# Performance work log

Hardware: AMD Instinct MI355X
Metric: run time of the kernel (lower is better)

The kernel has to match this reference:

```python
import jax, jax.numpy as jnp
import numpy as np

B, S, D_IN, D_A, L = 4, 4000, 1024, 512, 8921


def setup_inputs() -> dict:
    key = jax.random.key(0)
    ks = jax.random.split(key, 6)
    scale_w = 1.0 / np.sqrt(D_IN)
    scale_u = 1.0 / np.sqrt(D_A)
    return {
        "x": jax.random.normal(ks[0], (B, S, D_IN), jnp.float32),
        "W_w": jax.random.normal(ks[1], (D_A, D_IN), jnp.float32) * scale_w,
        "W_b": jax.random.normal(ks[2], (D_A,), jnp.float32) * 0.01,
        "U_w": jax.random.normal(ks[3], (L, D_A), jnp.float32) * scale_u,
        "V_w": jax.random.normal(ks[4], (L, D_A), jnp.float32) * scale_u,
        "V_b": jax.random.normal(ks[5], (L,), jnp.float32) * 0.01,
    }


def reference(x, W_w, W_b, U_w, V_w, V_b):
    # z = tanh(W x): [B, S, D_A]
    z = jnp.tanh(jnp.einsum("bsd,ad->bsa", x, W_w) + W_b)
    # label-wise attention scores over sequence: [B, L, S]
    scores = jnp.einsum("la,bsa->bls", U_w, z)
    alpha = jax.nn.softmax(scores, axis=-1)
    # per-label context vectors: [B, L, D_A]
    m = jnp.einsum("bls,bsa->bla", alpha, z)
    # per-label weighted dot-product classifier: [B, L]
    y = jnp.einsum("la,bla->bl", V_w, m) + V_b
    return (y, alpha)
```

## Files before the change

kernel.cpp:

```cpp
#include <hip/hip_runtime.h>
#include <hip/hip_bf16.h>
#include <math.h>

#define B_   4
#define S_   4000
#define DIN  1024
#define DA   512
#define L_   8921

typedef __attribute__((ext_vector_type(8))) short    short8;
typedef __attribute__((ext_vector_type(4))) float    f4;
typedef __attribute__((ext_vector_type(4))) unsigned int u4;

static __device__ __forceinline__ unsigned short f2b(float f) {
    unsigned int u = __float_as_uint(f);
    u += 0x7fffu + ((u >> 16) & 1u);
    return (unsigned short)(u >> 16);
}
static __device__ __forceinline__ unsigned int pack2(float lo, float hi) {
    return (unsigned int)f2b(lo) | ((unsigned int)f2b(hi) << 16);
}

__global__ __launch_bounds__(256) void k_z(const float* __restrict__ x,
                                           const float* __restrict__ Ww,
                                           const float* __restrict__ Wb,
                                           unsigned short* __restrict__ z)
{
    __shared__ unsigned short lds_a[128 * 32];
    __shared__ unsigned short lds_b[128 * 32];

    const int tid  = threadIdx.x;
    const int lane = tid & 63;
    const int w    = tid >> 6;
    const int wm   = w >> 1, wn = w & 1;
    const int q    = lane >> 4, r = lane & 15;
    const int m0   = blockIdx.x * 128;
    const int n0   = blockIdx.y * 128;

    f4 acc[4][4];
#pragma unroll
    for (int i = 0; i < 4; i++)
#pragma unroll
        for (int j = 0; j < 4; j++) { f4 zz = {0.f,0.f,0.f,0.f}; acc[i][j] = zz; }

    const int row  = tid >> 1;
    const int half = tid & 1;

    for (int kk = 0; kk < DIN; kk += 32) {
        {
            const f4* src = (const f4*)(x + (size_t)(m0 + row) * DIN + kk + half * 16);
            f4 v0 = src[0], v1 = src[1], v2 = src[2], v3 = src[3];
            u4* dst = (u4*)&lds_a[row * 32 + half * 16];
            u4 o0, o1;
            o0[0] = pack2(v0[0], v0[1]); o0[1] = pack2(v0[2], v0[3]);
            o0[2] = pack2(v1[0], v1[1]); o0[3] = pack2(v1[2], v1[3]);
            o1[0] = pack2(v2[0], v2[1]); o1[1] = pack2(v2[2], v2[3]);
            o1[2] = pack2(v3[0], v3[1]); o1[3] = pack2(v3[2], v3[3]);
            dst[0] = o0; dst[1] = o1;
        }
        {
            const f4* src = (const f4*)(Ww + (size_t)(n0 + row) * DIN + kk + half * 16);
            f4 v0 = src[0], v1 = src[1], v2 = src[2], v3 = src[3];
            u4* dst = (u4*)&lds_b[row * 32 + half * 16];
            u4 o0, o1;
            o0[0] = pack2(v0[0], v0[1]); o0[1] = pack2(v0[2], v0[3]);
            o0[2] = pack2(v1[0], v1[1]); o0[3] = pack2(v1[2], v1[3]);
            o1[0] = pack2(v2[0], v2[1]); o1[1] = pack2(v2[2], v2[3]);
            o1[2] = pack2(v3[0], v3[1]); o1[3] = pack2(v3[2], v3[3]);
            dst[0] = o0; dst[1] = o1;
        }
        __syncthreads();

        short8 af[4], bfr[4];
#pragma unroll
        for (int i = 0; i < 4; i++) {
            af[i]  = *(const short8*)&lds_a[(wm * 64 + i * 16 + r) * 32 + q * 8];
            bfr[i] = *(const short8*)&lds_b[(wn * 64 + i * 16 + r) * 32 + q * 8];
        }
#pragma unroll
        for (int i = 0; i < 4; i++)
#pragma unroll
            for (int j = 0; j < 4; j++)
                acc[i][j] = __builtin_amdgcn_mfma_f32_16x16x32_bf16(af[i], bfr[j], acc[i][j], 0, 0, 0);
        __syncthreads();
    }

#pragma unroll
    for (int i = 0; i < 4; i++) {
#pragma unroll
        for (int j = 0; j < 4; j++) {
            const int col = n0 + wn * 64 + j * 16 + r;
            const float bias = Wb[col];
#pragma unroll
            for (int e = 0; e < 4; e++) {
                const int rowg = m0 + wm * 64 + i * 16 + q * 4 + e;
                z[(size_t)rowg * DA + col] = f2b(tanhf(acc[i][j][e] + bias));
            }
        }
    }
}

__global__ __launch_bounds__(256) void k_scores(const float* __restrict__ U,
                                                const unsigned short* __restrict__ z,
                                                float* __restrict__ out)
{
    __shared__ unsigned short lds_a[128 * 32];
    __shared__ unsigned short lds_b[128 * 32];

    const int tid  = threadIdx.x;
    const int lane = tid & 63;
    const int w    = tid >> 6;
    const int wm   = w >> 1, wn = w & 1;
    const int q    = lane >> 4, r = lane & 15;
    const int b    = blockIdx.z;
    const int m0   = blockIdx.x * 128;
    const int n0   = blockIdx.y * 128;

    f4 acc[4][4];
#pragma unroll
    for (int i = 0; i < 4; i++)
#pragma unroll
        for (int j = 0; j < 4; j++) { f4 zz = {0.f,0.f,0.f,0.f}; acc[i][j] = zz; }

    const int row  = tid >> 1;
    const int half = tid & 1;
    const int brow = tid >> 2;
    const int bseg = tid & 3;

    for (int kk = 0; kk < DA; kk += 32) {
        {
            u4* dst = (u4*)&lds_a[row * 32 + half * 16];
            const int gm = m0 + row;
            if (gm < L_) {
                const f4* src = (const f4*)(U + (size_t)gm * DA + kk + half * 16);
                f4 v0 = src[0], v1 = src[1], v2 = src[2], v3 = src[3];
                u4 o0, o1;
                o0[0] = pack2(v0[0], v0[1]); o0[1] = pack2(v0[2], v0[3]);
                o0[2] = pack2(v1[0], v1[1]); o0[3] = pack2(v1[2], v1[3]);
                o1[0] = pack2(v2[0], v2[1]); o1[1] = pack2(v2[2], v2[3]);
                o1[2] = pack2(v3[0], v3[1]); o1[3] = pack2(v3[2], v3[3]);
                dst[0] = o0; dst[1] = o1;
            } else {
                u4 zz = {0,0,0,0}; dst[0] = zz; dst[1] = zz;
            }
        }
#pragma unroll
        for (int jj = 0; jj < 2; jj++) {
            const int rr = brow + jj * 64;
            const int gs = n0 + rr;
            u4* dst = (u4*)&lds_b[rr * 32 + bseg * 8];
            if (gs < S_) {
                *dst = *(const u4*)&z[((size_t)(b * S_ + gs)) * DA + kk + bseg * 8];
            } else {
                u4 zz = {0,0,0,0}; *dst = zz;
            }
        }
        __syncthreads();

        short8 af[4], bfr[4];
#pragma unroll
        for (int i = 0; i < 4; i++) {
            af[i]  = *(const short8*)&lds_a[(wm * 64 + i * 16 + r) * 32 + q * 8];
            bfr[i] = *(const short8*)&lds_b[(wn * 64 + i * 16 + r) * 32 + q * 8];
        }
#pragma unroll
        for (int i = 0; i < 4; i++)
#pragma unroll
            for (int j = 0; j < 4; j++)
                acc[i][j] = __builtin_amdgcn_mfma_f32_16x16x32_bf16(af[i], bfr[j], acc[i][j], 0, 0, 0);
        __syncthreads();
    }

#pragma unroll
    for (int i = 0; i < 4; i++) {
#pragma unroll
        for (int j = 0; j < 4; j++) {
            const int colg = n0 + wn * 64 + j * 16 + r;
#pragma unroll
            for (int e = 0; e < 4; e++) {
                const int rowg = m0 + wm * 64 + i * 16 + q * 4 + e;
                if (rowg < L_ && colg < S_)
                    out[((size_t)b * L_ + rowg) * S_ + colg] = acc[i][j][e];
            }
        }
    }
}

__global__ __launch_bounds__(256) void k_softmax(float* __restrict__ a)
{
    float* p = a + (size_t)blockIdx.x * S_;
    const int tid = threadIdx.x;

    f4 v[4];
    float mx = -3.4e38f;
#pragma unroll
    for (int j = 0; j < 4; j++) {
        const int vi = tid + j * 256;
        if (vi < S_ / 4) {
            v[j] = ((const f4*)p)[vi];
            mx = fmaxf(mx, fmaxf(fmaxf(v[j][0], v[j][1]), fmaxf(v[j][2], v[j][3])));
        }
    }
#pragma unroll
    for (int off = 32; off > 0; off >>= 1) mx = fmaxf(mx, __shfl_xor(mx, off, 64));

    __shared__ float red[8];
    if ((tid & 63) == 0) red[tid >> 6] = mx;
    __syncthreads();
    mx = fmaxf(fmaxf(red[0], red[1]), fmaxf(red[2], red[3]));

    float s = 0.f;
#pragma unroll
    for (int j = 0; j < 4; j++) {
        const int vi = tid + j * 256;
        if (vi < S_ / 4) {
#pragma unroll
            for (int c = 0; c < 4; c++) { v[j][c] = __expf(v[j][c] - mx); s += v[j][c]; }
        }
    }
#pragma unroll
    for (int off = 32; off > 0; off >>= 1) s += __shfl_xor(s, off, 64);
    if ((tid & 63) == 0) red[4 + (tid >> 6)] = s;
    __syncthreads();
    s = red[4] + red[5] + red[6] + red[7];

    const float inv = 1.f / s;
#pragma unroll
    for (int j = 0; j < 4; j++) {
        const int vi = tid + j * 256;
        if (vi < S_ / 4) {
            f4 o = v[j]; o[0] *= inv; o[1] *= inv; o[2] *= inv; o[3] *= inv;
            ((f4*)p)[vi] = o;
        }
    }
}

__global__ __launch_bounds__(256) void k_transpose(const unsigned short* __restrict__ z,
                                                   unsigned short* __restrict__ zT)
{
    __shared__ unsigned short t[32][33];
    const int b  = blockIdx.z;
    const int s0 = blockIdx.x * 32;
    const int a0 = blockIdx.y * 32;
    const int c  = threadIdx.x & 31;
    const int r4 = threadIdx.x >> 5;

#pragma unroll
    for (int i = 0; i < 4; i++) {
        const int sl = r4 * 4 + i;
        t[sl][c] = z[((size_t)(b * S_ + s0 + sl)) * DA + a0 + c];
    }
    __syncthreads();
#pragma unroll
    for (int i = 0; i < 4; i++) {
        const int al = r4 * 4 + i;
        zT[((size_t)(b * DA + a0 + al)) * S_ + s0 + c] = t[c][al];
    }
}

__global__ __launch_bounds__(256) void k_mv(const float* __restrict__ alpha,
                                            const unsigned short* __restrict__ zT,
                                            const float* __restrict__ Vw,
                                            const float* __restrict__ Vb,
                                            float* __restrict__ y)
{
    __shared__ unsigned short lds_a[64 * 32];
    __shared__ unsigned short lds_b[512 * 32];
    __shared__ float yred[64];

    const int tid  = threadIdx.x;
    const int lane = tid & 63;
    const int w    = tid >> 6;
    const int q    = lane >> 4, r = lane & 15;
    const int b    = blockIdx.y;
    const int m0   = blockIdx.x * 64;

    if (tid < 64) yred[tid] = 0.f;

    f4 acc[4][8];
#pragma unroll
    for (int i = 0; i < 4; i++)
#pragma unroll
        for (int j = 0; j < 8; j++) { f4 zz = {0.f,0.f,0.f,0.f}; acc[i][j] = zz; }

    const int arow = tid >> 2;
    const int aseg = tid & 3;

    for (int kk = 0; kk < S_; kk += 32) {
        {
            u4* dst = (u4*)&lds_a[arow * 32 + aseg * 8];
            const int gl = m0 + arow;
            if (gl < L_) {
                const f4* src = (const f4*)(alpha + ((size_t)b * L_ + gl) * S_ + kk + aseg * 8);
                f4 v0 = src[0], v1 = src[1];
                u4 o;
                o[0] = pack2(v0[0], v0[1]); o[1] = pack2(v0[2], v0[3]);
                o[2] = pack2(v1[0], v1[1]); o[3] = pack2(v1[2], v1[3]);
                *dst = o;
            } else {
                u4 zz = {0,0,0,0}; *dst = zz;
            }
        }
#pragma unroll
        for (int jj = 0; jj < 8; jj++) {
            const int rr = arow + jj * 64;
            *(u4*)&lds_b[rr * 32 + aseg * 8] =
                *(const u4*)&zT[((size_t)(b * DA + rr)) * S_ + kk + aseg * 8];
        }
        __syncthreads();

        short8 af[4], bfr[8];
#pragma unroll
        for (int i = 0; i < 4; i++)
            af[i] = *(const short8*)&lds_a[(i * 16 + r) * 32 + q * 8];
#pragma unroll
        for (int j = 0; j < 8; j++)
            bfr[j] = *(const short8*)&lds_b[(w * 128 + j * 16 + r) * 32 + q * 8];
#pragma unroll
        for (int i = 0; i < 4; i++)
#pragma unroll
            for (int j = 0; j < 8; j++)
                acc[i][j] = __builtin_amdgcn_mfma_f32_16x16x32_bf16(af[i], bfr[j], acc[i][j], 0, 0, 0);
        __syncthreads();
    }

#pragma unroll
    for (int i = 0; i < 4; i++) {
#pragma unroll
        for (int e = 0; e < 4; e++) {
            const int rowl = i * 16 + q * 4 + e;
            const int gl = m0 + rowl;
            if (gl < L_) {
                float p = 0.f;
#pragma unroll
                for (int j = 0; j < 8; j++) {
                    const int col = w * 128 + j * 16 + r;
                    p += acc[i][j][e] * Vw[(size_t)gl * DA + col];
                }
                atomicAdd(&yred[rowl], p);
            }
        }
    }
    __syncthreads();
    if (tid < 64 && (m0 + tid) < L_)
        y[b * L_ + m0 + tid] = yred[tid] + Vb[m0 + tid];
}

extern "C" void kernel_launch(void* const* d_in, const int* in_sizes, int n_in,
                              void* d_out, int out_size, void* d_ws, size_t ws_size,
                              hipStream_t stream)
{
    const float* x  = (const float*)d_in[0];
    const float* Ww = (const float*)d_in[1];
    const float* Wb = (const float*)d_in[2];
    const float* Uw = (const float*)d_in[3];
    const float* Vw = (const float*)d_in[4];
    const float* Vb = (const float*)d_in[5];

    float* y     = (float*)d_out;
    float* alpha = y + (size_t)B_ * L_;

    unsigned short* z  = (unsigned short*)d_ws;
    unsigned short* zT = z + (size_t)B_ * S_ * DA;

    k_z<<<dim3(125, 4), dim3(256), 0, stream>>>(x, Ww, Wb, z);
    k_scores<<<dim3(70, 32, B_), dim3(256), 0, stream>>>(Uw, z, alpha);
    k_softmax<<<dim3(B_ * L_), dim3(256), 0, stream>>>(alpha);
    k_transpose<<<dim3(125, 16, B_), dim3(256), 0, stream>>>(z, zT);
    k_mv<<<dim3(140, B_), dim3(256), 0, stream>>>(alpha, zT, Vw, Vb, y);
}
```

Before: 1.942 ms.

## Compute y via V·z scores and fuse softmax with the weighted reduction

The label outputs are rewritten algebraically as y[l] = Σ_s alpha[l,s]·(V_l·z_s) instead of first forming the context vectors m = alpha·z. A new GEMM kernel computes the U·z scores and the V·z products together, sharing the z tile loads, with U and V converted to bf16 beforehand. A fused kernel then does the softmax and the weighted sum over s in one pass, which removes the transpose and matrix-vector kernels. The catch is a full B×L×S intermediate (fp32, or bf16 as a fallback) that must be written and read back. This path only runs when the workspace is large enough; otherwise the old kernels are used.

```diff
diff --git a/kernel.cpp b/kernel.cpp
--- a/kernel.cpp
+++ b/kernel.cpp
@@ -8,9 +8,10 @@
 #define DA   512
 #define L_   8921
 
-typedef __attribute__((ext_vector_type(8))) short    short8;
-typedef __attribute__((ext_vector_type(4))) float    f4;
-typedef __attribute__((ext_vector_type(4))) unsigned int u4;
+typedef __attribute__((ext_vector_type(8))) short          short8;
+typedef __attribute__((ext_vector_type(4))) float          f4;
+typedef __attribute__((ext_vector_type(4))) unsigned int   u4;
+typedef __attribute__((ext_vector_type(4))) unsigned short us4;
 
 static __device__ __forceinline__ unsigned short f2b(float f) {
     unsigned int u = __float_as_uint(f);
@@ -19,6 +20,9 @@
 }
 static __device__ __forceinline__ unsigned int pack2(float lo, float hi) {
     return (unsigned int)f2b(lo) | ((unsigned int)f2b(hi) << 16);
+}
+static __device__ __forceinline__ float b2f(unsigned short u) {
+    return __uint_as_float(((unsigned int)u) << 16);
 }
 
 __global__ __launch_bounds__(256) void k_z(const float* __restrict__ x,
@@ -97,6 +101,180 @@
                 z[(size_t)rowg * DA + col] = f2b(tanhf(acc[i][j][e] + bias));
             }
         }
+    }
+}
+
+__global__ __launch_bounds__(256) void k_cvt(const float* __restrict__ src,
+                                             unsigned short* __restrict__ dst, int n8)
+{
+    const int i = blockIdx.x * 256 + threadIdx.x;
+    if (i < n8) {
+        const f4* s = (const f4*)src + (size_t)i * 2;
+        const f4 a = s[0], b = s[1];
+        u4 o;
+        o[0] = pack2(a[0], a[1]); o[1] = pack2(a[2], a[3]);
+        o[2] = pack2(b[0], b[1]); o[3] = pack2(b[2], b[3]);
+        *((u4*)dst + i) = o;
+    }
+}
+
+template<bool TB16>
+__global__ __launch_bounds__(256) void k_uv(const unsigned short* __restrict__ Ubf,
+                                            const unsigned short* __restrict__ Vbf,
+                                            const unsigned short* __restrict__ z,
+                                            float* __restrict__ scores,
+                                            void* __restrict__ Tout)
+{
+    __shared__ unsigned short lds_u[128 * 32];
+    __shared__ unsigned short lds_v[128 * 32];
+    __shared__ unsigned short lds_z[128 * 32];
+
+    const int tid  = threadIdx.x;
+    const int lane = tid & 63;
+    const int w    = tid >> 6;
+    const int wm   = w >> 1, wn = w & 1;
+    const int q    = lane >> 4, r = lane & 15;
+    const int b    = blockIdx.z;
+    const int m0   = blockIdx.x * 128;
+    const int n0   = blockIdx.y * 128;
+
+    f4 accU[4][4], accV[4][4];
+#pragma unroll
+    for (int i = 0; i < 4; i++)
+#pragma unroll
+        for (int j = 0; j < 4; j++) {
+            f4 zz = {0.f,0.f,0.f,0.f};
+            accU[i][j] = zz; accV[i][j] = zz;
+        }
+
+    const int srow = tid >> 2;
+    const int sseg = tid & 3;
+
+    for (int kk = 0; kk < DA; kk += 32) {
+#pragma unroll
+        for (int jj = 0; jj < 2; jj++) {
+            const int rr = srow + jj * 64;
+            const int gm = m0 + rr;
+            const int gs = n0 + rr;
+            u4 zz = {0,0,0,0};
+            u4 vu = zz, vv = zz, vz = zz;
+            if (gm < L_) {
+                vu = *(const u4*)&Ubf[(size_t)gm * DA + kk + sseg * 8];
+                vv = *(const u4*)&Vbf[(size_t)gm * DA + kk + sseg * 8];
+            }
+            if (gs < S_) {
+                vz = *(const u4*)&z[((size_t)(b * S_ + gs)) * DA + kk + sseg * 8];
+            }
+            *(u4*)&lds_u[rr * 32 + sseg * 8] = vu;
+            *(u4*)&lds_v[rr * 32 + sseg * 8] = vv;
+            *(u4*)&lds_z[rr * 32 + sseg * 8] = vz;
+        }
+        __syncthreads();
+
+        short8 fu[4], fv[4], fz[4];
+#pragma unroll
+        for (int i = 0; i < 4; i++) {
+            fu[i] = *(const short8*)&lds_u[(wm * 64 + i * 16 + r) * 32 + q * 8];
+            fv[i] = *(const short8*)&lds_v[(wm * 64 + i * 16 + r) * 32 + q * 8];
+            fz[i] = *(const short8*)&lds_z[(wn * 64 + i * 16 + r) * 32 + q * 8];
+        }
+#pragma unroll
+        for (int i = 0; i < 4; i++)
+#pragma unroll
+            for (int j = 0; j < 4; j++) {
+                accU[i][j] = __builtin_amdgcn_mfma_f32_16x16x32_bf16(fu[i], fz[j], accU[i][j], 0, 0, 0);
+                accV[i][j] = __builtin_amdgcn_mfma_f32_16x16x32_bf16(fv[i], fz[j], accV[i][j], 0, 0, 0);
+            }
+        __syncthreads();
+    }
+
+#pragma unroll
+    for (int i = 0; i < 4; i++) {
+#pragma unroll
+        for (int j = 0; j < 4; j++) {
+            const int colg = n0 + wn * 64 + j * 16 + r;
+#pragma unroll
+            for (int e = 0; e < 4; e++) {
+                const int rowg = m0 + wm * 64 + i * 16 + q * 4 + e;
+                if (rowg < L_ && colg < S_) {
+                    const size_t idx = ((size_t)b * L_ + rowg) * S_ + colg;
+                    scores[idx] = accU[i][j][e];
+                    if constexpr (TB16) ((unsigned short*)Tout)[idx] = f2b(accV[i][j][e]);
+                    else                ((float*)Tout)[idx]          = accV[i][j][e];
+                }
+            }
+        }
+    }
+}
+
+template<bool TB16>
+__global__ __launch_bounds__(256) void k_fsy(float* __restrict__ sc,
+                                             const void* __restrict__ Tin,
+                                             const float* __restrict__ Vbias,
+                                             float* __restrict__ y)
+{
+    const size_t rb = (size_t)blockIdx.x * S_;
+    float* p = sc + rb;
+    const int tid = threadIdx.x;
+
+    f4 v[4];
+    float mx = -3.4e38f;
+#pragma unroll
+    for (int j = 0; j < 4; j++) {
+        const int vi = tid + j * 256;
+        if (vi < S_ / 4) {
+            v[j] = ((const f4*)p)[vi];
+            mx = fmaxf(mx, fmaxf(fmaxf(v[j][0], v[j][1]), fmaxf(v[j][2], v[j][3])));
+        }
+    }
+#pragma unroll
+    for (int off = 32; off > 0; off >>= 1) mx = fmaxf(mx, __shfl_xor(mx, off, 64));
+
+    __shared__ float red[12];
+    if ((tid & 63) == 0) red[tid >> 6] = mx;
+    __syncthreads();
+    mx = fmaxf(fmaxf(red[0], red[1]), fmaxf(red[2], red[3]));
+
+    float s = 0.f;
+#pragma unroll
+    for (int j = 0; j < 4; j++) {
+        const int vi = tid + j * 256;
+        if (vi < S_ / 4) {
+#pragma unroll
+            for (int c = 0; c < 4; c++) { v[j][c] = __expf(v[j][c] - mx); s += v[j][c]; }
+        }
+    }
+#pragma unroll
+    for (int off = 32; off > 0; off >>= 1) s += __shfl_xor(s, off, 64);
+    if ((tid & 63) == 0) red[4 + (tid >> 6)] = s;
+    __syncthreads();
+    s = red[4] + red[5] + red[6] + red[7];
+    const float inv = 1.f / s;
+
+    float yp = 0.f;
+#pragma unroll
+    for (int j = 0; j < 4; j++) {
+        const int vi = tid + j * 256;
+        if (vi < S_ / 4) {
+            f4 o = v[j];
+            o[0] *= inv; o[1] *= inv; o[2] *= inv; o[3] *= inv;
+            ((f4*)p)[vi] = o;
+            if constexpr (TB16) {
+                const us4 tv = ((const us4*)((const unsigned short*)Tin + rb))[vi];
+                yp += o[0] * b2f(tv[0]) + o[1] * b2f(tv[1]) + o[2] * b2f(tv[2]) + o[3] * b2f(tv[3]);
+            } else {
+                const f4 tv = ((const f4*)((const float*)Tin + rb))[vi];
+                yp += o[0] * tv[0] + o[1] * tv[1] + o[2] * tv[2] + o[3] * tv[3];
+            }
+        }
+    }
+#pragma unroll
+    for (int off = 32; off > 0; off >>= 1) yp += __shfl_xor(yp, off, 64);
+    if ((tid & 63) == 0) red[8 + (tid >> 6)] = yp;
+    __syncthreads();
+    if (tid == 0) {
+        const int l = (int)(blockIdx.x % (unsigned)L_);
+        y[blockIdx.x] = red[8] + red[9] + red[10] + red[11] + Vbias[l];
     }
 }
 
@@ -360,12 +538,38 @@
     float* y     = (float*)d_out;
     float* alpha = y + (size_t)B_ * L_;
 
-    unsigned short* z  = (unsigned short*)d_ws;
-    unsigned short* zT = z + (size_t)B_ * S_ * DA;
+    unsigned short* z = (unsigned short*)d_ws;
+    const size_t z_bytes  = (size_t)B_ * S_ * DA * 2;
+    const size_t uv_bytes = (size_t)L_ * DA * 2;
+    unsigned short* Ubf = (unsigned short*)((char*)d_ws + z_bytes);
+    unsigned short* Vbf = (unsigned short*)((char*)d_ws + z_bytes + uv_bytes);
+    char* Tp = (char*)d_ws + z_bytes + 2 * uv_bytes;
+    const size_t T_f32 = (size_t)B_ * L_ * S_ * 4;
+    const size_t T_b16 = (size_t)B_ * L_ * S_ * 2;
+    const size_t need_f32 = z_bytes + 2 * uv_bytes + T_f32;
+    const size_t need_b16 = z_bytes + 2 * uv_bytes + T_b16;
 
     k_z<<<dim3(125, 4), dim3(256), 0, stream>>>(x, Ww, Wb, z);
-    k_scores<<<dim3(70, 32, B_), dim3(256), 0, stream>>>(Uw, z, alpha);
-    k_softmax<<<dim3(B_ * L_), dim3(256), 0, stream>>>(alpha);
-    k_transpose<<<dim3(125, 16, B_), dim3(256), 0, stream>>>(z, zT);
-    k_mv<<<dim3(140, B_), dim3(256), 0, stream>>>(alpha, zT, Vw, Vb, y);
-}
+
+    if (ws_size >= need_f32) {
+        const int n8 = (L_ * DA) / 8;
+        const int gc = (n8 + 255) / 256;
+        k_cvt<<<dim3(gc), dim3(256), 0, stream>>>(Uw, Ubf, n8);
+        k_cvt<<<dim3(gc), dim3(256), 0, stream>>>(Vw, Vbf, n8);
+        k_uv<false><<<dim3(70, 32, B_), dim3(256), 0, stream>>>(Ubf, Vbf, z, alpha, (void*)Tp);
+        k_fsy<false><<<dim3(B_ * L_), dim3(256), 0, stream>>>(alpha, (const void*)Tp, Vb, y);
+    } else if (ws_size >= need_b16) {
+        const int n8 = (L_ * DA) / 8;
+        const int gc = (n8 + 255) / 256;
+        k_cvt<<<dim3(gc), dim3(256), 0, stream>>>(Uw, Ubf, n8);
+        k_cvt<<<dim3(gc), dim3(256), 0, stream>>>(Vw, Vbf, n8);
+        k_uv<true><<<dim3(70, 32, B_), dim3(256), 0, stream>>>(Ubf, Vbf, z, alpha, (void*)Tp);
+        k_fsy<true><<<dim3(B_ * L_), dim3(256), 0, stream>>>(alpha, (const void*)Tp, Vb, y);
+    } else {
+        unsigned short* zT = z + (size_t)B_ * S_ * DA;
+        k_scores<<<dim3(70, 32, B_), dim3(256), 0, stream>>>(Uw, z, alpha);
+        k_softmax<<<dim3(B_ * L_), dim3(256), 0, stream>>>(alpha);
+        k_transpose<<<dim3(125, 16, B_), dim3(256), 0, stream>>>(z, zT);
+        k_mv<<<dim3(140, B_), dim3(256), 0, stream>>>(alpha, zT, Vw, Vb, y);
+    }
+}
```

After: 1.696 ms. 1.14x faster.
